# Performance work log

Hardware: AMD Instinct MI355X
Metric: run time of the kernel (lower is better)

Reference implementation:

```python
import jax, jax.numpy as jnp
import numpy as np


def setup_inputs() -> dict:
    key = jax.random.key(0)
    k1, k2 = jax.random.split(key)
    B, F, E, U = 16384, 39, 64, 128
    embeds = jax.random.normal(k1, (B, F, E), dtype=jnp.float32)
    outer_w = jax.random.normal(k2, (U, E, E), dtype=jnp.float32) * 0.05
    return {"embeds": embeds, "outer_w": outer_w}


def reference(embeds, outer_w):
    # embeds: (B, F, E) = concatenated field embeddings; outer_w: (U, E, E)
    feat_sum = jnp.sum(embeds, axis=1)  # (B, E)
    # lp[b,u] = sum_{i,j} feat_sum[b,i] * feat_sum[b,j] * outer_w[u,i,j]
    # == f^T W_u f, computed as a batched GEMM instead of the original's
    # per-unit elementwise multiply+reduce loop (same math).
    fw = jnp.einsum('bi,uij->buj', feat_sum, outer_w)  # (B, U, E)
    lp = jnp.einsum('buj,bj->bu', fw, feat_sum)        # (B, U)
    return lp
```

## Files before the change

kernel.cpp:

```cpp
#include <hip/hip_runtime.h>

#define B_TOTAL 16384
#define F 39
#define E 64
#define U 128
#define BT 64
#define THREADS 512

typedef __attribute__((ext_vector_type(8))) short short8;
typedef __attribute__((ext_vector_type(4))) float f32x4;
typedef __attribute__((ext_vector_type(4))) unsigned u32x4;

__device__ __forceinline__ unsigned pack2_bf16(float a, float b) {
  unsigned ua = __builtin_bit_cast(unsigned, a) + 0x8000u;
  unsigned ub = __builtin_bit_cast(unsigned, b) + 0x8000u;
  return (ub & 0xFFFF0000u) | (ua >> 16);
}

__global__ __launch_bounds__(256) void prep_w(const float* __restrict__ w,
                                              u32x4* __restrict__ wf) {
  int tid = blockIdx.x * 256 + threadIdx.x;
  int lane = tid & 63;
  int frag = tid >> 6;
  int ks  = frag & 1;
  int ntg = (frag >> 1) & 7;
  int i   = frag >> 4;
  int uu  = ntg * 16 + (lane & 15);
  int k0  = ks * 32 + (lane >> 4) * 8;
  const f32x4* src = (const f32x4*)(w + (size_t)uu * (E * E) + i * E + k0);
  f32x4 v0 = __builtin_nontemporal_load(src);
  f32x4 v1 = __builtin_nontemporal_load(src + 1);
  u32x4 o;
  o[0] = pack2_bf16(v0[0], v0[1]);
  o[1] = pack2_bf16(v0[2], v0[3]);
  o[2] = pack2_bf16(v1[0], v1[1]);
  o[3] = pack2_bf16(v1[2], v1[3]);
  wf[tid] = o;
}

__global__ __launch_bounds__(THREADS) void fused_outer(
    const float* __restrict__ embeds, const u32x4* __restrict__ wf,
    float* __restrict__ out) {
  __shared__ __align__(16) float Ft[BT * 68];
  __shared__ __align__(16) float FtT[E * 68];

  const int t = threadIdx.x;
  const int b0 = blockIdx.x * BT;

  #pragma unroll
  for (int task = t; task < BT * 16; task += THREADS) {
    int b = task >> 4, e4 = task & 15;
    const f32x4* src = (const f32x4*)(embeds + (size_t)(b0 + b) * (F * E)) + e4;
    f32x4 s = {0.f, 0.f, 0.f, 0.f};
    #pragma unroll
    for (int f = 0; f < F; ++f) {
      f32x4 v = __builtin_nontemporal_load(src + f * (E / 4));
      s += v;
    }
    *(f32x4*)&Ft[b * 68 + e4 * 4] = s;
    FtT[(e4 * 4 + 0) * 68 + b] = s[0];
    FtT[(e4 * 4 + 1) * 68 + b] = s[1];
    FtT[(e4 * 4 + 2) * 68 + b] = s[2];
    FtT[(e4 * 4 + 3) * 68 + b] = s[3];
  }

  const int lane = t & 63, wave = t >> 6;
  const int fl = lane & 15;
  const int fo = (lane >> 4) * 8;
  const int r0 = (lane >> 4) * 4;

  const u32x4* wv = wf + (size_t)(wave * 2) * 64 + lane;

  #define LOADW(buf, ii) {                 \
    buf[0] = wv[(size_t)((ii) * 16) * 64]; \
    buf[1] = wv[(size_t)((ii) * 16 + 1) * 64]; }

  u32x4 w0[2], w1[2], w2[2], w3[2];
  LOADW(w0, 0);
  LOADW(w1, 1);
  LOADW(w2, 2);
  LOADW(w3, 3);
  __syncthreads();

  short8 af[4][2];
  #pragma unroll
  for (int mt = 0; mt < 4; ++mt) {
    const float* fr = &Ft[(mt * 16 + fl) * 68];
    #pragma unroll
    for (int ks = 0; ks < 2; ++ks) {
      f32x4 v0 = *(const f32x4*)&fr[ks * 32 + fo];
      f32x4 v1 = *(const f32x4*)&fr[ks * 32 + fo + 4];
      u32x4 o;
      o[0] = pack2_bf16(v0[0], v0[1]);
      o[1] = pack2_bf16(v0[2], v0[3]);
      o[2] = pack2_bf16(v1[0], v1[1]);
      o[3] = pack2_bf16(v1[2], v1[3]);
      af[mt][ks] = __builtin_bit_cast(short8, o);
    }
  }

  f32x4 acc[4];
  #pragma unroll
  for (int mt = 0; mt < 4; ++mt)
    #pragma unroll
    for (int r = 0; r < 4; ++r) acc[mt][r] = 0.f;

  #define STEP(ii, buf) {                                                      \
    short8 bf0 = __builtin_bit_cast(short8, buf[0]);                           \
    short8 bf1 = __builtin_bit_cast(short8, buf[1]);                           \
    _Pragma("unroll")                                                          \
    for (int mt = 0; mt < 4; ++mt) {                                           \
      f32x4 s = {0.f, 0.f, 0.f, 0.f};                                          \
      s = __builtin_amdgcn_mfma_f32_16x16x32_bf16(af[mt][0], bf0, s, 0, 0, 0); \
      s = __builtin_amdgcn_mfma_f32_16x16x32_bf16(af[mt][1], bf1, s, 0, 0, 0); \
      f32x4 fi = *(const f32x4*)&FtT[(ii) * 68 + mt * 16 + r0];                \
      acc[mt] += fi * s;                                                       \
    } }

  for (int i = 0; i < E; i += 4) {
    STEP(i, w0);     LOADW(w0, i + 4);
    STEP(i + 1, w1); LOADW(w1, i + 5);
    STEP(i + 2, w2); LOADW(w2, i + 6);
    STEP(i + 3, w3); LOADW(w3, i + 7);
  }

  #pragma unroll
  for (int mt = 0; mt < 4; ++mt)
    #pragma unroll
    for (int r = 0; r < 4; ++r)
      __builtin_nontemporal_store(
          acc[mt][r],
          &out[(size_t)(b0 + mt * 16 + r0 + r) * U + wave * 16 + fl]);
  #undef LOADW
  #undef STEP
}

extern "C" void kernel_launch(void* const* d_in, const int* in_sizes, int n_in,
                              void* d_out, int out_size, void* d_ws, size_t ws_size,
                              hipStream_t stream) {
  const float* embeds = (const float*)d_in[0];
  const float* w      = (const float*)d_in[1];
  float* out          = (float*)d_out;
  u32x4* wf           = (u32x4*)d_ws;
  prep_w<<<dim3(256), dim3(256), 0, stream>>>(w, wf);
  fused_outer<<<dim3(B_TOTAL / BT), dim3(THREADS), 0, stream>>>(embeds, wf, out);
}
```

Measured before the change: 236.0 us.

## Split the i-reduction across two wave groups with a shared-memory partial-sum combine

Doubles the block to 1024 threads. Each group of 8 waves handles half of the i dimension (32 rows of W) for the same 16-unit column slices, so each wave runs half as many MFMA steps. The second half writes its partial accumulators into shared memory, which reuses the Ft buffer after an added barrier, and the first half adds them before storing the output. This shortens the serial dependency chain per wave and gives more waves per CU to hide latency. The cost is two extra barriers, a shared-memory round trip for the partials, and register pressure under the 1024-thread launch bound.

```diff
diff --git a/kernel.cpp b/kernel.cpp
--- a/kernel.cpp
+++ b/kernel.cpp
@@ -5,7 +5,7 @@
 #define E 64
 #define U 128
 #define BT 64
-#define THREADS 512
+#define THREADS 1024
 
 typedef __attribute__((ext_vector_type(8))) short short8;
 typedef __attribute__((ext_vector_type(4))) float f32x4;
@@ -41,22 +41,21 @@
 __global__ __launch_bounds__(THREADS) void fused_outer(
     const float* __restrict__ embeds, const u32x4* __restrict__ wf,
     float* __restrict__ out) {
-  __shared__ __align__(16) float Ft[BT * 68];
+  __shared__ __align__(16) char smem0[32768];
   __shared__ __align__(16) float FtT[E * 68];
+  float* Ft  = (float*)smem0;
+  f32x4* prt = (f32x4*)smem0;
 
   const int t = threadIdx.x;
   const int b0 = blockIdx.x * BT;
 
-  #pragma unroll
-  for (int task = t; task < BT * 16; task += THREADS) {
-    int b = task >> 4, e4 = task & 15;
+  {
+    const int b = t >> 4, e4 = t & 15;
     const f32x4* src = (const f32x4*)(embeds + (size_t)(b0 + b) * (F * E)) + e4;
     f32x4 s = {0.f, 0.f, 0.f, 0.f};
     #pragma unroll
-    for (int f = 0; f < F; ++f) {
-      f32x4 v = __builtin_nontemporal_load(src + f * (E / 4));
-      s += v;
-    }
+    for (int f = 0; f < F; ++f)
+      s += __builtin_nontemporal_load(src + f * (E / 4));
     *(f32x4*)&Ft[b * 68 + e4 * 4] = s;
     FtT[(e4 * 4 + 0) * 68 + b] = s[0];
     FtT[(e4 * 4 + 1) * 68 + b] = s[1];
@@ -65,21 +64,24 @@
   }
 
   const int lane = t & 63, wave = t >> 6;
+  const int uc = wave & 7;
+  const int kh = wave >> 3;
   const int fl = lane & 15;
   const int fo = (lane >> 4) * 8;
   const int r0 = (lane >> 4) * 4;
 
-  const u32x4* wv = wf + (size_t)(wave * 2) * 64 + lane;
+  const u32x4* wv = wf + (size_t)(uc * 2) * 64 + lane;
 
   #define LOADW(buf, ii) {                 \
     buf[0] = wv[(size_t)((ii) * 16) * 64]; \
     buf[1] = wv[(size_t)((ii) * 16 + 1) * 64]; }
 
+  const int i0 = kh * 32;
   u32x4 w0[2], w1[2], w2[2], w3[2];
-  LOADW(w0, 0);
-  LOADW(w1, 1);
-  LOADW(w2, 2);
-  LOADW(w3, 3);
+  LOADW(w0, i0);
+  LOADW(w1, i0 + 1);
+  LOADW(w2, i0 + 2);
+  LOADW(w3, i0 + 3);
   __syncthreads();
 
   short8 af[4][2];
@@ -98,6 +100,7 @@
       af[mt][ks] = __builtin_bit_cast(short8, o);
     }
   }
+  __syncthreads();
 
   f32x4 acc[4];
   #pragma unroll
@@ -117,20 +120,29 @@
       acc[mt] += fi * s;                                                       \
     } }
 
-  for (int i = 0; i < E; i += 4) {
+  for (int i = i0; i < i0 + 32; i += 4) {
     STEP(i, w0);     LOADW(w0, i + 4);
     STEP(i + 1, w1); LOADW(w1, i + 5);
     STEP(i + 2, w2); LOADW(w2, i + 6);
     STEP(i + 3, w3); LOADW(w3, i + 7);
   }
 
-  #pragma unroll
-  for (int mt = 0; mt < 4; ++mt)
+  if (kh == 1) {
     #pragma unroll
-    for (int r = 0; r < 4; ++r)
-      __builtin_nontemporal_store(
-          acc[mt][r],
-          &out[(size_t)(b0 + mt * 16 + r0 + r) * U + wave * 16 + fl]);
+    for (int mt = 0; mt < 4; ++mt)
+      prt[(uc * 64 + lane) * 4 + mt] = acc[mt];
+  }
+  __syncthreads();
+  if (kh == 0) {
+    #pragma unroll
+    for (int mt = 0; mt < 4; ++mt) {
+      f32x4 v = acc[mt] + prt[(uc * 64 + lane) * 4 + mt];
+      #pragma unroll
+      for (int r = 0; r < 4; ++r)
+        __builtin_nontemporal_store(
+            v[r], &out[(size_t)(b0 + mt * 16 + r0 + r) * U + uc * 16 + fl]);
+    }
+  }
   #undef LOADW
   #undef STEP
 }
```

Result: no change. 233.0 us (-1.3%).
